# Optimization experiments

Hardware: AMD Instinct MI355X
Metric: run time of the kernel (lower is better)

Reference implementation:

```python
import jax, jax.numpy as jnp
import numpy as np
from jax import lax

B, DIM, H, W = 8, 256, 48, 48
HEADS, DH = 8, 32
K, S = 5, 2
P = K // 2
SCALE = DH ** -0.5
EPS = 1e-5


def setup_inputs() -> dict:
    key = jax.random.key(0)
    ks = jax.random.split(key, 12)
    w = lambda k, sh: jax.random.normal(k, sh, jnp.float32) * 0.02
    return {
        'x': jax.random.normal(ks[0], (B, DIM, H, W), jnp.float32),
        'kv': jax.random.normal(ks[1], (B, DIM, H, W), jnp.float32),
        'wq': w(ks[2], (DIM, DIM)), 'bq': jnp.zeros((DIM,), jnp.float32),
        'wk': w(ks[3], (DIM, DIM)), 'bk': jnp.zeros((DIM,), jnp.float32),
        'wv': w(ks[4], (DIM, DIM)), 'bv': jnp.zeros((DIM,), jnp.float32),
        'w_dw': w(ks[5], (DH, 1, K, K)), 'b_dw': jnp.zeros((DH,), jnp.float32),
        'ln_w': jnp.ones((DH,), jnp.float32), 'ln_b': jnp.zeros((DH,), jnp.float32),
        'w_off': w(ks[6], (2, DH)),
        'wo': w(ks[7], (DIM, DIM)), 'bo': jnp.zeros((DIM,), jnp.float32),
    }


def conv1x1(x, w, b=None):
    # x: (B, Cin, H, W), w: (Cout, Cin)
    y = jnp.einsum('oc,bchw->bohw', w, x)
    return y if b is None else y + b[None, :, None, None]


def grid_sample_bilinear(inp, grid):
    # inp: (N, C, Hh, Ww); grid: (N, Hg, Wg, 2) in (x, y), align_corners=True
    N, C, Hh, Ww = inp.shape
    gx = (grid[..., 0] + 1.0) * 0.5 * (Ww - 1)
    gy = (grid[..., 1] + 1.0) * 0.5 * (Hh - 1)
    x0 = jnp.floor(gx)
    y0 = jnp.floor(gy)
    wx = gx - x0  # frac weights for x1/y1 corners
    wy = gy - y0
    x0i = jnp.clip(x0.astype(jnp.int32), 0, Ww - 1)
    x1i = jnp.clip(x0.astype(jnp.int32) + 1, 0, Ww - 1)
    y0i = jnp.clip(y0.astype(jnp.int32), 0, Hh - 1)
    y1i = jnp.clip(y0.astype(jnp.int32) + 1, 0, Hh - 1)
    flat = inp.reshape(N, C, Hh * Ww)
    n = grid.shape[1] * grid.shape[2]

    def gather(yi, xi):
        idx = (yi * Ww + xi).reshape(N, 1, n)
        return jnp.take_along_axis(flat, jnp.broadcast_to(idx, (N, C, n)), axis=2)

    w00 = ((1 - wx) * (1 - wy)).reshape(N, 1, n)
    w01 = (wx * (1 - wy)).reshape(N, 1, n)
    w10 = ((1 - wx) * wy).reshape(N, 1, n)
    w11 = (wx * wy).reshape(N, 1, n)
    return (w00 * gather(y0i, x0i) + w01 * gather(y0i, x1i)
            + w10 * gather(y1i, x0i) + w11 * gather(y1i, x1i))  # (N, C, n)


def reference(x, kv, wq, bq, wk, bk, wv, bv, w_dw, b_dw, ln_w, ln_b, w_off, wo, bo):
    q = conv1x1(x, wq, bq)                      # (B, DIM, H, W)
    q_off = q.reshape(B * HEADS, DH, H, W)      # per-head channels
    # depthwise offset conv
    t = lax.conv_general_dilated(q_off, w_dw, (S, S), [(P, P), (P, P)],
                                 feature_group_count=DH,
                                 dimension_numbers=('NCHW', 'OIHW', 'NCHW'))
    t = t + b_dw[None, :, None, None]
    Hk, Wk = t.shape[2], t.shape[3]
    n = Hk * Wk
    # LayerNormProxy: LN over channel dim
    t = t.transpose(0, 2, 3, 1)                 # (BH, Hk, Wk, DH)
    mu = t.mean(-1, keepdims=True)
    var = ((t - mu) ** 2).mean(-1, keepdims=True)
    t = (t - mu) / jnp.sqrt(var + EPS) * ln_w + ln_b
    t = jax.nn.gelu(t, approximate=False)
    offset = jnp.einsum('oc,bhwc->bhwo', w_off, t)  # (BH, Hk, Wk, 2) as (y, x)
    # reference points, normalized to [-1, 1]
    ref_y = (jnp.linspace(0.5, Hk - 0.5, Hk, dtype=jnp.float32) / (Hk - 1.0)) * 2.0 - 1.0
    ref_x = (jnp.linspace(0.5, Wk - 0.5, Wk, dtype=jnp.float32) / (Wk - 1.0)) * 2.0 - 1.0
    ref = jnp.stack(jnp.meshgrid(ref_y, ref_x, indexing='ij'), axis=-1)  # (Hk, Wk, 2)
    pos = jnp.clip(offset + ref[None], -1.0, 1.0)
    grid = pos[..., ::-1]                       # (x, y) order for sampling
    kvs = grid_sample_bilinear(kv.reshape(B * HEADS, DH, H, W), grid)  # (BH, DH, n)
    kv4 = kvs.reshape(B, DIM, 1, n)
    k = conv1x1(kv4, wk, bk).reshape(B * HEADS, DH, n)
    v = conv1x1(kv4, wv, bv).reshape(B * HEADS, DH, n)
    qf = q.reshape(B * HEADS, DH, H * W)
    attn = jax.nn.softmax(jnp.einsum('bcm,bcn->bmn', qf, k) * SCALE, axis=2)
    out = jnp.einsum('bmn,bcn->bcm', attn, v).reshape(B, DIM, H, W)
    return conv1x1(out, wo, bo)
```

## Files before the change

kernel.cpp:

```cpp
#include <hip/hip_runtime.h>
#include <hip/hip_bf16.h>
#include <cstddef>

#define BB 8
#define DIM 256
#define HH 48
#define WW 48
#define HW 2304
#define HEADS 8
#define DH 32
#define BH 64
#define HK 24
#define WK 24
#define NN 576
#define SCALE 0.17677669529663687f
#define EPSF 1e-5f

typedef __attribute__((ext_vector_type(8))) short short8;
typedef __attribute__((ext_vector_type(4))) float f32x4;

static __device__ inline short f2bf_s(float f) {
  __hip_bfloat16 h = __float2bfloat16(f);
  return *reinterpret_cast<short*>(&h);
}

static __device__ inline unsigned pkrnd(float a, float b) {
  unsigned ua = __builtin_bit_cast(unsigned, a) + 0x8000u;
  unsigned ub = __builtin_bit_cast(unsigned, b) + 0x8000u;
  return __builtin_amdgcn_perm(ub, ua, 0x07060302);
}

__global__ __launch_bounds__(256) void prep(
    const float* __restrict__ x, const float* __restrict__ wq,
    short* __restrict__ Xh, short* __restrict__ Xl,
    short* __restrict__ Wqh, short* __restrict__ Wql) {
  __shared__ float t[64][65];
  const int bid = blockIdx.x;
  if (bid < 1152) {
    int mt = bid % 36, t2 = bid / 36;
    int ct = t2 & 3, b = t2 >> 2;
    const int c0 = ct * 64, m0 = mt * 64;
    const int col = threadIdx.x & 63, row4 = threadIdx.x >> 6;
    const float* xb = x + ((size_t)b * 256 + c0) * HW + m0;
#pragma unroll
    for (int k = 0; k < 16; k++) {
      int c = row4 + k * 4;
      t[c][col] = xb[(size_t)c * HW + col];
    }
    __syncthreads();
    short* oh = Xh + ((size_t)b * HW + m0) * 256 + c0;
    short* ol = Xl + ((size_t)b * HW + m0) * 256 + c0;
#pragma unroll
    for (int k = 0; k < 16; k++) {
      int m = row4 + k * 4;
      float v = t[col][m];
      unsigned u = __builtin_bit_cast(unsigned, v) & 0xffff0000u;
      float rem = v - __builtin_bit_cast(float, u);
      oh[(size_t)m * 256 + col] = (short)(u >> 16);
      ol[(size_t)m * 256 + col] = (short)(__builtin_bit_cast(unsigned, rem) >> 16);
    }
  } else {
    int e0 = (bid - 1152) * 1024 + threadIdx.x * 4;
    float4 v4 = *(const float4*)(wq + e0);
    float vv[4] = {v4.x, v4.y, v4.z, v4.w};
    union { short s[4]; int2 i2; } Hu, Lu;
#pragma unroll
    for (int j = 0; j < 4; j++) {
      unsigned u = __builtin_bit_cast(unsigned, vv[j]) & 0xffff0000u;
      float rem = vv[j] - __builtin_bit_cast(float, u);
      Hu.s[j] = (short)(u >> 16);
      Lu.s[j] = (short)(__builtin_bit_cast(unsigned, rem) >> 16);
    }
    *(int2*)(Wqh + e0) = Hu.i2;
    *(int2*)(Wql + e0) = Lu.i2;
  }
}

__global__ __launch_bounds__(512) void gemm_q_fused(
    const short* __restrict__ Wh, const short* __restrict__ Wl,
    const float* __restrict__ bias,
    const short* __restrict__ Xh, const short* __restrict__ Xl,
    float* __restrict__ Y,
    const float* __restrict__ kv, float* __restrict__ kvT,
    const float* __restrict__ wk, const float* __restrict__ wv,
    const float* __restrict__ wo,
    short* __restrict__ Wkh, short* __restrict__ Wkl,
    short* __restrict__ Wvh, short* __restrict__ Wvl,
    short* __restrict__ Woh, short* __restrict__ Wol) {
  __shared__ short sB[2][64 * 256];
  const int bid = blockIdx.x;
  const int tid = threadIdx.x;

  if (bid < 288) {
    const int b = bid / 36;
    const int mBase = (bid % 36) * 64;
    const short* srcH = Xh + ((size_t)b * HW + mBase) * 256;
    const short* srcL = Xl + ((size_t)b * HW + mBase) * 256;
#pragma unroll
    for (int it = 0; it < 4; it++) {
      int idx = it * 512 + tid;
      int row = idx >> 5, ck = idx & 31;
      int dst = row * 256 + ((ck ^ (row & 7)) << 3);
      *(short8*)(&sB[0][dst]) = *(const short8*)(srcH + (size_t)row * 256 + ck * 8);
      *(short8*)(&sB[1][dst]) = *(const short8*)(srcL + (size_t)row * 256 + ck * 8);
    }
    __syncthreads();

    const int wave = tid >> 6, lane = tid & 63;
    const int quad = lane >> 4, l15 = lane & 15;
    const int oBase = wave * 32;
    f32x4 acc[2][4] = {};
    for (int kc = 0; kc < 256; kc += 32) {
      short8 ah[2], al[2];
#pragma unroll
      for (int os = 0; os < 2; os++) {
        ah[os] = *(const short8*)(Wh + (size_t)(oBase + os * 16 + l15) * 256 + kc + quad * 8);
        al[os] = *(const short8*)(Wl + (size_t)(oBase + os * 16 + l15) * 256 + kc + quad * 8);
      }
#pragma unroll
      for (int mt = 0; mt < 4; mt++) {
        int row = mt * 16 + l15;
        int off = row * 256 + ((((kc >> 3) + quad) ^ (row & 7)) << 3);
        short8 bh_ = *(const short8*)(&sB[0][off]);
        short8 bl_ = *(const short8*)(&sB[1][off]);
#pragma unroll
        for (int os = 0; os < 2; os++) {
          acc[os][mt] = __builtin_amdgcn_mfma_f32_16x16x32_bf16(ah[os], bh_, acc[os][mt], 0, 0, 0);
          acc[os][mt] = __builtin_amdgcn_mfma_f32_16x16x32_bf16(al[os], bh_, acc[os][mt], 0, 0, 0);
          acc[os][mt] = __builtin_amdgcn_mfma_f32_16x16x32_bf16(ah[os], bl_, acc[os][mt], 0, 0, 0);
        }
      }
    }
#pragma unroll
    for (int os = 0; os < 2; os++)
#pragma unroll
      for (int r = 0; r < 4; r++) {
        int o = oBase + os * 16 + quad * 4 + r;
        float bs = bias[o];
        float* yp = Y + ((size_t)b * 256 + o) * HW + mBase + l15;
#pragma unroll
        for (int mt = 0; mt < 4; mt++) yp[mt * 16] = acc[os][mt][r] + bs;
      }
  } else if (bid < 1440) {
    float* tf = (float*)sB;
    int bb = bid - 288;
    int mt = bb % 36, t2 = bb / 36;
    int ct = t2 & 3, b = t2 >> 2;
    const int c0 = ct * 64, m0 = mt * 64;
    const int col = tid & 63, row8 = tid >> 6;
    const float* xb = kv + ((size_t)b * 256 + c0) * HW + m0;
#pragma unroll
    for (int k = 0; k < 8; k++) {
      int c = row8 + k * 8;
      tf[c * 65 + col] = xb[(size_t)c * HW + col];
    }
    __syncthreads();
    float* ot = kvT + ((size_t)b * HW + m0) * 256 + c0;
#pragma unroll
    for (int k = 0; k < 8; k++) {
      int m = row8 + k * 8;
      ot[(size_t)m * 256 + col] = tf[col * 65 + m];
    }
  } else {
    const float* srcs[3] = {wk, wv, wo};
    short* his[3] = {Wkh, Wvh, Woh};
    short* los[3] = {Wkl, Wvl, Wol};
    int bb = bid - 1440;
    int w = bb >> 5;
    int off = (bb & 31) * 2048 + tid * 4;
    float4 v4 = *(const float4*)(srcs[w] + off);
    float vv[4] = {v4.x, v4.y, v4.z, v4.w};
    union { short s[4]; int2 i2; } Hu, Lu;
#pragma unroll
    for (int j = 0; j < 4; j++) {
      unsigned u = __builtin_bit_cast(unsigned, vv[j]) & 0xffff0000u;
      float rem = vv[j] - __builtin_bit_cast(float, u);
      Hu.s[j] = (short)(u >> 16);
      Lu.s[j] = (short)(__builtin_bit_cast(unsigned, rem) >> 16);
    }
    *(int2*)(his[w] + off) = Hu.i2;
    *(int2*)(los[w] + off) = Lu.i2;
  }
}

#define QPS 101
__global__ __launch_bounds__(256) void dw_sample_kernel(
    const float* __restrict__ q, const float* __restrict__ kvT,
    const float* __restrict__ w_dw, const float* __restrict__ b_dw,
    const float* __restrict__ ln_w, const float* __restrict__ ln_b,
    const float* __restrict__ w_off, short* __restrict__ kvsTh,
    short* __restrict__ kvsTl) {
  __shared__ float s_q[32 * QPS];
  __shared__ float s_w[DH * 25];
  const int tid = threadIdx.x;
  const int ch = tid & 31;
  const int np = tid >> 5;
  const int bid = blockIdx.x;
  const int b = bid & 7;
  const int r = bid >> 3;
  const int head = r / 72;
  const int rr = r - head * 72;
  const int yk = rr / 3;
  const int xk0 = (rr - yk * 3) * 8;
  const int bh = b * 8 + head;
  const int xk = xk0 + np;
  const int n = yk * WK + xk;

  for (int i = tid; i < DH * 25; i += 256) s_w[i] = w_dw[i];

  {
    const int y0 = yk * 2 - 2, x0 = xk0 * 2 - 2;
    const float* qbh = q + (size_t)bh * DH * HW;
#pragma unroll
    for (int it = 0; it < 13; it++) {
      int e = it * 256 + tid;
      if (e < 3200) {
        int c = e / 100;
        int rem = e - c * 100;
        int dy = rem / 20;
        int xl = rem - dy * 20;
        int gy = y0 + dy, gx = x0 + xl;
        float v = 0.f;
        if ((unsigned)gy < HH && (unsigned)gx < WW)
          v = qbh[(size_t)c * HW + gy * WW + gx];
        s_q[c * QPS + dy * 20 + xl] = v;
      }
    }
  }
  __syncthreads();

  float t = b_dw[ch];
  {
    const float* wp = s_w + ch * 25;
    const float* qp = s_q + ch * QPS + np * 2;
#pragma unroll
    for (int dy = 0; dy < 5; dy++)
#pragma unroll
      for (int dx = 0; dx < 5; dx++)
        t += wp[dy * 5 + dx] * qp[dy * 20 + dx];
  }

  float mu = t;
#pragma unroll
  for (int m = 1; m < 32; m <<= 1) mu += __shfl_xor(mu, m);
  mu *= (1.0f / DH);
  float d = t - mu;
  float var = d * d;
#pragma unroll
  for (int m = 1; m < 32; m <<= 1) var += __shfl_xor(var, m);
  var *= (1.0f / DH);
  float rstd = rsqrtf(var + EPSF);

  float xn = d * rstd * ln_w[ch] + ln_b[ch];
  float g = 0.5f * xn * (1.0f + erff(xn * 0.70710678118654752f));
  float o0 = w_off[ch] * g;
  float o1 = w_off[DH + ch] * g;
#pragma unroll
  for (int m = 1; m < 32; m <<= 1) {
    o0 += __shfl_xor(o0, m);
    o1 += __shfl_xor(o1, m);
  }

  const float ref_y = (0.5f + (float)yk) / 23.0f * 2.0f - 1.0f;
  const float ref_x = (0.5f + (float)xk) / 23.0f * 2.0f - 1.0f;
  float py = fminf(fmaxf(o0 + ref_y, -1.0f), 1.0f);
  float px = fminf(fmaxf(o1 + ref_x, -1.0f), 1.0f);

  float gx = (px + 1.0f) * 0.5f * 47.0f;
  float gy = (py + 1.0f) * 0.5f * 47.0f;
  float x0f = floorf(gx), y0f = floorf(gy);
  float wx = gx - x0f, wy = gy - y0f;
  int x0 = (int)x0f, y0 = (int)y0f;
  int x0i = min(max(x0, 0), WW - 1);
  int x1i = min(max(x0 + 1, 0), WW - 1);
  int y0i = min(max(y0, 0), HH - 1);
  int y1i = min(max(y0 + 1, 0), HH - 1);
  float w00 = (1.f - wx) * (1.f - wy);
  float w01 = wx * (1.f - wy);
  float w10 = (1.f - wx) * wy;
  float w11 = wx * wy;

  const float* kvb = kvT + (size_t)b * HW * 256 + head * DH + ch;
  float val = w00 * kvb[(size_t)(y0i * WW + x0i) * 256]
            + w01 * kvb[(size_t)(y0i * WW + x1i) * 256]
            + w10 * kvb[(size_t)(y1i * WW + x0i) * 256]
            + w11 * kvb[(size_t)(y1i * WW + x1i) * 256];

  unsigned ub = __builtin_bit_cast(unsigned, val);
  unsigned uh = ub & 0xffff0000u;
  float rem = val - __builtin_bit_cast(float, uh);
  size_t idx = ((size_t)b * NN + n) * 256 + head * DH + ch;
  kvsTh[idx] = (short)(uh >> 16);
  kvsTl[idx] = (short)(__builtin_bit_cast(unsigned, rem) >> 16);
}

__global__ __launch_bounds__(256) void kv_gemm_mfma(
    const short* __restrict__ Wkh, const short* __restrict__ Wkl,
    const float* __restrict__ bk,
    const short* __restrict__ Wvh, const short* __restrict__ Wvl,
    const float* __restrict__ bv,
    const short* __restrict__ Xh, const short* __restrict__ Xl,
    short* __restrict__ Kb, short* __restrict__ Vb) {
  const int tid = threadIdx.x;
  const int wave = tid >> 6;
  const int lane = tid & 63;
  const int quad = lane >> 4, l15 = lane & 15;
  const int b = blockIdx.z;
  const int mode = blockIdx.y >> 2;
  const int oTile = (blockIdx.y & 3) * 64;
  const int nBase = blockIdx.x * 64;

  if (mode == 0) {
    const int nW = nBase + wave * 16;
    const short* arh = Xh + ((size_t)b * NN + nW + l15) * 256 + quad * 8;
    const short* arl = Xl + ((size_t)b * NN + nW + l15) * 256 + quad * 8;
    f32x4 acc[4] = {};
    for (int kc = 0; kc < 256; kc += 32) {
      short8 ah = *(const short8*)(arh + kc);
      short8 al = *(const short8*)(arl + kc);
#pragma unroll
      for (int ot = 0; ot < 4; ot++) {
        short8 bh_ = *(const short8*)(Wkh + (size_t)(oTile + ot * 16 + l15) * 256 + kc + quad * 8);
        short8 bl_ = *(const short8*)(Wkl + (size_t)(oTile + ot * 16 + l15) * 256 + kc + quad * 8);
        acc[ot] = __builtin_amdgcn_mfma_f32_16x16x32_bf16(ah, bh_, acc[ot], 0, 0, 0);
        acc[ot] = __builtin_amdgcn_mfma_f32_16x16x32_bf16(al, bh_, acc[ot], 0, 0, 0);
        acc[ot] = __builtin_amdgcn_mfma_f32_16x16x32_bf16(ah, bl_, acc[ot], 0, 0, 0);
      }
    }
    float bs[4];
#pragma unroll
    for (int ot = 0; ot < 4; ot++) bs[ot] = bk[oTile + ot * 16 + l15];
#pragma unroll
    for (int r = 0; r < 4; r++) {
      short* yp = Kb + ((size_t)b * NN + nW + quad * 4 + r) * 256 + oTile + l15;
#pragma unroll
      for (int ot = 0; ot < 4; ot++) yp[ot * 16] = f2bf_s(acc[ot][r] + bs[ot]);
    }
  } else {
    const int oW = oTile + wave * 16;
    const short* arh = Wvh + (size_t)(oW + l15) * 256 + quad * 8;
    const short* arl = Wvl + (size_t)(oW + l15) * 256 + quad * 8;
    f32x4 acc[4] = {};
    for (int kc = 0; kc < 256; kc += 32) {
      short8 ah = *(const short8*)(arh + kc);
      short8 al = *(const short8*)(arl + kc);
#pragma unroll
      for (int nt = 0; nt < 4; nt++) {
        short8 bh_ = *(const short8*)(Xh + ((size_t)b * NN + nBase + nt * 16 + l15) * 256 + kc + quad * 8);
        short8 bl_ = *(const short8*)(Xl + ((size_t)b * NN + nBase + nt * 16 + l15) * 256 + kc + quad * 8);
        acc[nt] = __builtin_amdgcn_mfma_f32_16x16x32_bf16(ah, bh_, acc[nt], 0, 0, 0);
        acc[nt] = __builtin_amdgcn_mfma_f32_16x16x32_bf16(al, bh_, acc[nt], 0, 0, 0);
        acc[nt] = __builtin_amdgcn_mfma_f32_16x16x32_bf16(ah, bl_, acc[nt], 0, 0, 0);
      }
    }
#pragma unroll
    for (int r = 0; r < 4; r++) {
      int o = oW + quad * 4 + r;
      float bs = bv[o];
      short* yp = Vb + ((size_t)b * 256 + o) * NN + nBase + l15;
#pragma unroll
      for (int nt = 0; nt < 4; nt++) yp[nt * 16] = f2bf_s(acc[nt][r] + bs);
    }
  }
}

__global__ __launch_bounds__(256) void attn_mfma(const float* __restrict__ q,
                                                 const short* __restrict__ Kb,
                                                 const short* __restrict__ Vb,
                                                 short* __restrict__ O) {
  __shared__ short sK[2][64 * 40];
  __shared__ short sV[2][32 * 88];
  __shared__ int sP[4][2][256];
  const int tid = threadIdx.x;
  const int wave = tid >> 6;
  const int lane = tid & 63;
  const int quad = lane >> 4;
  const int l15 = lane & 15;
  const int bh = blockIdx.y;
  const int b = bh >> 3, head = bh & 7;
  const int mBase = blockIdx.x * 128 + wave * 32;

  short8 bq[2];
#pragma unroll
  for (int mt = 0; mt < 2; mt++) {
    const float* qp = q + ((size_t)bh * DH + quad * 8) * HW + mBase + mt * 16 + l15;
    short8 v;
#pragma unroll
    for (int j = 0; j < 8; j++) v[j] = f2bf_s(qp[(size_t)j * HW] * SCALE);
    bq[mt] = v;
  }

  const int kn = tid >> 2, kc = (tid & 3) * 8;
  const int vc = tid >> 3, vn = (tid & 7) * 8;
  const short* kg = Kb + (size_t)b * NN * 256 + head * DH;
  const short* vg = Vb + ((size_t)b * 256 + head * DH) * NN;

  short8 kreg = *(const short8*)(kg + (size_t)kn * 256 + kc);
  short8 vreg = *(const short8*)(vg + (size_t)vc * NN + vn);
  *(short8*)(&sK[0][kn * 40 + kc]) = kreg;
  *(short8*)(&sV[0][vc * 88 + vn]) = vreg;
  __syncthreads();

  const int g = (l15 >> 1) & 3;
  const int row16 = l15 * 16;
  const int wr0 = row16 + (((quad >> 1) ^ g) << 2) + ((quad & 1) << 1);
  const int wr1 = row16 + (((2 + (quad >> 1)) ^ g) << 2) + ((quad & 1) << 1);
  const int rd = row16 + ((quad ^ g) << 2);

  f32x4 oacc[2][2] = {};
  f32x4 dacc[2] = {};
  const short ONE = 0x3F80;
  const short8 ones = {ONE, ONE, ONE, ONE, ONE, ONE, ONE, ONE};

  for (int s = 0; s < 9; s++) {
    const int buf = s & 1;
    if (s + 1 < 9) {
      kreg = *(const short8*)(kg + (size_t)((s + 1) * 64 + kn) * 256 + kc);
      vreg = *(const short8*)(vg + (size_t)vc * NN + (s + 1) * 64 + vn);
    }
#pragma unroll
    for (int nt = 0; nt < 2; nt++) {
      short8 ka0 = *(const short8*)(&sK[buf][(nt * 32 + l15) * 40 + quad * 8]);
      short8 ka1 = *(const short8*)(&sK[buf][(nt * 32 + 16 + l15) * 40 + quad * 8]);
      short8 va0 = *(const short8*)(&sV[buf][l15 * 88 + nt * 32 + quad * 8]);
      short8 va1 = *(const short8*)(&sV[buf][(16 + l15) * 88 + nt * 32 + quad * 8]);
      f32x4 z = {0.f, 0.f, 0.f, 0.f};
      f32x4 st[2][2];
      st[0][0] = __builtin_amdgcn_mfma_f32_16x16x32_bf16(ka0, bq[0], z, 0, 0, 0);
      st[0][1] = __builtin_amdgcn_mfma_f32_16x16x32_bf16(ka1, bq[0], z, 0, 0, 0);
      st[1][0] = __builtin_amdgcn_mfma_f32_16x16x32_bf16(ka0, bq[1], z, 0, 0, 0);
      st[1][1] = __builtin_amdgcn_mfma_f32_16x16x32_bf16(ka1, bq[1], z, 0, 0, 0);
#pragma unroll
      for (int mt = 0; mt < 2; mt++) {
        float p0 = __expf(st[mt][0][0]), p1 = __expf(st[mt][0][1]);
        float p2 = __expf(st[mt][0][2]), p3 = __expf(st[mt][0][3]);
        float p4 = __expf(st[mt][1][0]), p5 = __expf(st[mt][1][1]);
        float p6 = __expf(st[mt][1][2]), p7 = __expf(st[mt][1][3]);
        int* base = &sP[wave][mt][0];
        *(int2*)(base + wr0) = make_int2((int)pkrnd(p0, p1), (int)pkrnd(p2, p3));
        *(int2*)(base + wr1) = make_int2((int)pkrnd(p4, p5), (int)pkrnd(p6, p7));
      }
#pragma unroll
      for (int mt = 0; mt < 2; mt++) {
        short8 pa = *(short8*)(&sP[wave][mt][0] + rd);
        oacc[mt][0] = __builtin_amdgcn_mfma_f32_16x16x32_bf16(pa, va0, oacc[mt][0], 0, 0, 0);
        oacc[mt][1] = __builtin_amdgcn_mfma_f32_16x16x32_bf16(pa, va1, oacc[mt][1], 0, 0, 0);
        dacc[mt] = __builtin_amdgcn_mfma_f32_16x16x32_bf16(pa, ones, dacc[mt], 0, 0, 0);
      }
    }
    if (s + 1 < 9) {
      *(short8*)(&sK[buf ^ 1][kn * 40 + kc]) = kreg;
      *(short8*)(&sV[buf ^ 1][vc * 88 + vn]) = vreg;
    }
    __syncthreads();
  }

#pragma unroll
  for (int mt = 0; mt < 2; mt++) {
    short* ob = O + ((size_t)b * HW + mBase + mt * 16) * 256 + head * DH + l15;
#pragma unroll
    for (int r = 0; r < 4; r++) {
      float inv = 1.0f / dacc[mt][r];
      ob[(size_t)(quad * 4 + r) * 256] = f2bf_s(oacc[mt][0][r] * inv);
      ob[(size_t)(quad * 4 + r) * 256 + 16] = f2bf_s(oacc[mt][1][r] * inv);
    }
  }
}

__global__ __launch_bounds__(512) void wo_gemm_mfma(const short* __restrict__ Whi,
                                                    const short* __restrict__ Wlo,
                                                    const float* __restrict__ bias,
                                                    const short* __restrict__ X,
                                                    float* __restrict__ Y) {
  __shared__ short sX[64 * 256];
  const int tid = threadIdx.x;
  const int b = blockIdx.y;
  const int mBase = blockIdx.x * 64;

  const short* src = X + ((size_t)b * HW + mBase) * 256;
#pragma unroll
  for (int it = 0; it < 4; it++) {
    int idx = it * 512 + tid;
    int row = idx >> 5, ck = idx & 31;
    *(short8*)(&sX[row * 256 + ((ck ^ (row & 7)) << 3)]) =
        *(const short8*)(src + (size_t)row * 256 + ck * 8);
  }
  __syncthreads();

  const int wave = tid >> 6, lane = tid & 63;
  const int quad = lane >> 4, l15 = lane & 15;
  const int oBase = wave * 32;

  f32x4 acc[2][4] = {};
  for (int kc = 0; kc < 256; kc += 32) {
    short8 ah[2], al[2];
#pragma unroll
    for (int os = 0; os < 2; os++) {
      ah[os] = *(const short8*)(Whi + (size_t)(oBase + os * 16 + l15) * 256 + kc + quad * 8);
      al[os] = *(const short8*)(Wlo + (size_t)(oBase + os * 16 + l15) * 256 + kc + quad * 8);
    }
#pragma unroll
    for (int mt = 0; mt < 4; mt++) {
      int row = mt * 16 + l15;
      short8 bx = *(const short8*)(&sX[row * 256 + ((((kc >> 3) + quad) ^ (row & 7)) << 3)]);
#pragma unroll
      for (int os = 0; os < 2; os++) {
        acc[os][mt] = __builtin_amdgcn_mfma_f32_16x16x32_bf16(ah[os], bx, acc[os][mt], 0, 0, 0);
        acc[os][mt] = __builtin_amdgcn_mfma_f32_16x16x32_bf16(al[os], bx, acc[os][mt], 0, 0, 0);
      }
    }
  }

#pragma unroll
  for (int os = 0; os < 2; os++)
#pragma unroll
    for (int r = 0; r < 4; r++) {
      int o = oBase + os * 16 + quad * 4 + r;
      float bs = bias[o];
      float* yp = Y + ((size_t)b * 256 + o) * HW + mBase + l15;
#pragma unroll
      for (int mt = 0; mt < 4; mt++) yp[mt * 16] = acc[os][mt][r] + bs;
    }
}

extern "C" void kernel_launch(void* const* d_in, const int* in_sizes, int n_in,
                              void* d_out, int out_size, void* d_ws, size_t ws_size,
                              hipStream_t stream) {
  const float* x    = (const float*)d_in[0];
  const float* kv   = (const float*)d_in[1];
  const float* wq   = (const float*)d_in[2];
  const float* bq   = (const float*)d_in[3];
  const float* wk   = (const float*)d_in[4];
  const float* bk   = (const float*)d_in[5];
  const float* wv   = (const float*)d_in[6];
  const float* bv   = (const float*)d_in[7];
  const float* w_dw = (const float*)d_in[8];
  const float* b_dw = (const float*)d_in[9];
  const float* ln_w = (const float*)d_in[10];
  const float* ln_b = (const float*)d_in[11];
  const float* w_off= (const float*)d_in[12];
  const float* wo   = (const float*)d_in[13];
  const float* bo   = (const float*)d_in[14];
  float* out = (float*)d_out;
  float* ws = (float*)d_ws;

  float* q     = ws;
  short* Xth   = (short*)(ws + 4718592);
  short* O     = (short*)(ws + 4718592);
  short* Xtl   = (short*)(ws + 7077888);
  short* kvsTh = (short*)(ws + 7077888);
  short* kvsTl = (short*)(ws + 7667712);
  short* Kb    = (short*)(ws + 8257536);
  short* Vb    = (short*)(ws + 8847360);
  short* Wqh   = (short*)(ws + 9437184);
  short* Wql = Wqh + 65536;
  short* Wkh = Wql + 65536;
  short* Wkl = Wkh + 65536;
  short* Wvh = Wkl + 65536;
  short* Wvl = Wvh + 65536;
  short* Woh = Wvl + 65536;
  short* Wol = Woh + 65536;
  float* kvT = out;

  prep<<<dim3(1216), dim3(256), 0, stream>>>(x, wq, Xth, Xtl, Wqh, Wql);
  gemm_q_fused<<<dim3(1536), dim3(512), 0, stream>>>(
      Wqh, Wql, bq, Xth, Xtl, q,
      kv, kvT, wk, wv, wo, Wkh, Wkl, Wvh, Wvl, Woh, Wol);
  dw_sample_kernel<<<dim3(BH * NN / 8), dim3(256), 0, stream>>>(
      q, kvT, w_dw, b_dw, ln_w, ln_b, w_off, kvsTh, kvsTl);
  kv_gemm_mfma<<<dim3(NN / 64, 8, BB), dim3(256), 0, stream>>>(
      Wkh, Wkl, bk, Wvh, Wvl, bv, kvsTh, kvsTl, Kb, Vb);
  attn_mfma<<<dim3(HW / 128, BH), dim3(256), 0, stream>>>(q, Kb, Vb, O);
  wo_gemm_mfma<<<dim3(HW / 64, BB), dim3(512), 0, stream>>>(Woh, Wol, bo, O, out);
}
```

Baseline: 230.7 us.

## Fuse bf16 hi/lo splitting into GEMM kernels and drop prep kernel

Removes the separate prep kernel. The Q GEMM now reads fp32 x directly, transposes it and splits it into bf16 hi/lo in LDS in two channel halves, prefetching the second half while computing on the first. All weight matrices (wq, wk, wv, wo) are loaded as fp32 and split into hi/lo in registers inside the GEMM kernels instead of being pre-converted. This saves one launch and the round trip of the Xh/Xl intermediates through global memory, at the cost of redundant per-block weight conversion and doubled weight load bytes.

Result: faster. 222.0 us (-3.8%).

```diff
diff --git a/kernel.cpp b/kernel.cpp
--- a/kernel.cpp
+++ b/kernel.cpp
@@ -30,107 +30,113 @@
   return __builtin_amdgcn_perm(ub, ua, 0x07060302);
 }
 
-__global__ __launch_bounds__(256) void prep(
-    const float* __restrict__ x, const float* __restrict__ wq,
-    short* __restrict__ Xh, short* __restrict__ Xl,
-    short* __restrict__ Wqh, short* __restrict__ Wql) {
-  __shared__ float t[64][65];
-  const int bid = blockIdx.x;
-  if (bid < 1152) {
-    int mt = bid % 36, t2 = bid / 36;
-    int ct = t2 & 3, b = t2 >> 2;
-    const int c0 = ct * 64, m0 = mt * 64;
-    const int col = threadIdx.x & 63, row4 = threadIdx.x >> 6;
-    const float* xb = x + ((size_t)b * 256 + c0) * HW + m0;
-#pragma unroll
-    for (int k = 0; k < 16; k++) {
-      int c = row4 + k * 4;
-      t[c][col] = xb[(size_t)c * HW + col];
-    }
-    __syncthreads();
-    short* oh = Xh + ((size_t)b * HW + m0) * 256 + c0;
-    short* ol = Xl + ((size_t)b * HW + m0) * 256 + c0;
-#pragma unroll
-    for (int k = 0; k < 16; k++) {
-      int m = row4 + k * 4;
-      float v = t[col][m];
-      unsigned u = __builtin_bit_cast(unsigned, v) & 0xffff0000u;
-      float rem = v - __builtin_bit_cast(float, u);
-      oh[(size_t)m * 256 + col] = (short)(u >> 16);
-      ol[(size_t)m * 256 + col] = (short)(__builtin_bit_cast(unsigned, rem) >> 16);
-    }
-  } else {
-    int e0 = (bid - 1152) * 1024 + threadIdx.x * 4;
-    float4 v4 = *(const float4*)(wq + e0);
-    float vv[4] = {v4.x, v4.y, v4.z, v4.w};
-    union { short s[4]; int2 i2; } Hu, Lu;
-#pragma unroll
-    for (int j = 0; j < 4; j++) {
-      unsigned u = __builtin_bit_cast(unsigned, vv[j]) & 0xffff0000u;
-      float rem = vv[j] - __builtin_bit_cast(float, u);
-      Hu.s[j] = (short)(u >> 16);
-      Lu.s[j] = (short)(__builtin_bit_cast(unsigned, rem) >> 16);
-    }
-    *(int2*)(Wqh + e0) = Hu.i2;
-    *(int2*)(Wql + e0) = Lu.i2;
-  }
+static __device__ inline void split8(const float* xf, short8& bh, short8& bl) {
+  union { unsigned u[4]; short8 v; } H, L;
+#pragma unroll
+  for (int p = 0; p < 4; p++) {
+    float x0 = xf[2 * p], x1 = xf[2 * p + 1];
+    unsigned u0 = __builtin_bit_cast(unsigned, x0) & 0xffff0000u;
+    unsigned u1 = __builtin_bit_cast(unsigned, x1) & 0xffff0000u;
+    float l0 = x0 - __builtin_bit_cast(float, u0);
+    float l1 = x1 - __builtin_bit_cast(float, u1);
+    H.u[p] = __builtin_amdgcn_perm(u1, u0, 0x07060302);
+    L.u[p] = __builtin_amdgcn_perm(__builtin_bit_cast(unsigned, l1),
+                                   __builtin_bit_cast(unsigned, l0), 0x07060302);
+  }
+  bh = H.v;
+  bl = L.v;
 }
 
 __global__ __launch_bounds__(512) void gemm_q_fused(
-    const short* __restrict__ Wh, const short* __restrict__ Wl,
-    const float* __restrict__ bias,
-    const short* __restrict__ Xh, const short* __restrict__ Xl,
-    float* __restrict__ Y,
-    const float* __restrict__ kv, float* __restrict__ kvT,
-    const float* __restrict__ wk, const float* __restrict__ wv,
-    const float* __restrict__ wo,
-    short* __restrict__ Wkh, short* __restrict__ Wkl,
-    short* __restrict__ Wvh, short* __restrict__ Wvl,
-    short* __restrict__ Woh, short* __restrict__ Wol) {
-  __shared__ short sB[2][64 * 256];
+    const float* __restrict__ wq, const float* __restrict__ bias,
+    const float* __restrict__ x, float* __restrict__ Y,
+    const float* __restrict__ kv, float* __restrict__ kvT) {
+  __shared__ float sLDS[16384];
+  float* s_raw = sLDS;
+  short* s_h   = (short*)(sLDS + 8192);
+  short* s_l   = ((short*)(sLDS + 8192)) + 8192;
   const int bid = blockIdx.x;
   const int tid = threadIdx.x;
 
   if (bid < 288) {
     const int b = bid / 36;
     const int mBase = (bid % 36) * 64;
-    const short* srcH = Xh + ((size_t)b * HW + mBase) * 256;
-    const short* srcL = Xl + ((size_t)b * HW + mBase) * 256;
-#pragma unroll
-    for (int it = 0; it < 4; it++) {
-      int idx = it * 512 + tid;
-      int row = idx >> 5, ck = idx & 31;
-      int dst = row * 256 + ((ck ^ (row & 7)) << 3);
-      *(short8*)(&sB[0][dst]) = *(const short8*)(srcH + (size_t)row * 256 + ck * 8);
-      *(short8*)(&sB[1][dst]) = *(const short8*)(srcL + (size_t)row * 256 + ck * 8);
-    }
-    __syncthreads();
-
     const int wave = tid >> 6, lane = tid & 63;
     const int quad = lane >> 4, l15 = lane & 15;
     const int oBase = wave * 32;
+    const int cm = tid & 63, cg = tid >> 6;
+    const int ck0 = cg * 2, ck1 = cg * 2 + 1;
+    const int cvt0 = cm * 128 + ((ck0 ^ (cm & 7)) << 3);
+    const int cvt1 = cm * 128 + ((ck1 ^ (cm & 7)) << 3);
+
     f32x4 acc[2][4] = {};
-    for (int kc = 0; kc < 256; kc += 32) {
-      short8 ah[2], al[2];
-#pragma unroll
-      for (int os = 0; os < 2; os++) {
-        ah[os] = *(const short8*)(Wh + (size_t)(oBase + os * 16 + l15) * 256 + kc + quad * 8);
-        al[os] = *(const short8*)(Wl + (size_t)(oBase + os * 16 + l15) * 256 + kc + quad * 8);
-      }
-#pragma unroll
-      for (int mt = 0; mt < 4; mt++) {
-        int row = mt * 16 + l15;
-        int off = row * 256 + ((((kc >> 3) + quad) ^ (row & 7)) << 3);
-        short8 bh_ = *(const short8*)(&sB[0][off]);
-        short8 bl_ = *(const short8*)(&sB[1][off]);
+
+    {
+      const float* xb = x + ((size_t)b * 256) * HW + mBase;
+#pragma unroll
+      for (int it = 0; it < 4; it++) {
+        int u = it * 512 + tid;
+        int c = u >> 4, f4 = u & 15;
+        *(float4*)(&s_raw[c * 64 + f4 * 4]) =
+            *(const float4*)(xb + (size_t)c * HW + f4 * 4);
+      }
+    }
+    __syncthreads();
+
+    for (int half = 0; half < 2; half++) {
+      {
+        float vals[16];
+#pragma unroll
+        for (int i = 0; i < 16; i++) vals[i] = s_raw[(cg * 16 + i) * 64 + cm];
+        short8 h0, l0, h1, l1;
+        split8(vals, h0, l0);
+        split8(vals + 8, h1, l1);
+        *(short8*)(&s_h[cvt0]) = h0;
+        *(short8*)(&s_l[cvt0]) = l0;
+        *(short8*)(&s_h[cvt1]) = h1;
+        *(short8*)(&s_l[cvt1]) = l1;
+      }
+      __syncthreads();
+
+      if (half == 0) {
+        const float* xb = x + ((size_t)b * 256 + 128) * HW + mBase;
+#pragma unroll
+        for (int it = 0; it < 4; it++) {
+          int u = it * 512 + tid;
+          int c = u >> 4, f4 = u & 15;
+          *(float4*)(&s_raw[c * 64 + f4 * 4]) =
+              *(const float4*)(xb + (size_t)c * HW + f4 * 4);
+        }
+      }
+
+      for (int kc = 0; kc < 128; kc += 32) {
+        short8 ah[2], al[2];
 #pragma unroll
         for (int os = 0; os < 2; os++) {
-          acc[os][mt] = __builtin_amdgcn_mfma_f32_16x16x32_bf16(ah[os], bh_, acc[os][mt], 0, 0, 0);
-          acc[os][mt] = __builtin_amdgcn_mfma_f32_16x16x32_bf16(al[os], bh_, acc[os][mt], 0, 0, 0);
-          acc[os][mt] = __builtin_amdgcn_mfma_f32_16x16x32_bf16(ah[os], bl_, acc[os][mt], 0, 0, 0);
+          const float* wrow = wq + (size_t)(oBase + os * 16 + l15) * 256 +
+                              half * 128 + kc + quad * 8;
+          float w8[8];
+          *(float4*)(w8) = *(const float4*)(wrow);
+          *(float4*)(w8 + 4) = *(const float4*)(wrow + 4);
+          split8(w8, ah[os], al[os]);
         }
-      }
-    }
+#pragma unroll
+        for (int mt = 0; mt < 4; mt++) {
+          int row = mt * 16 + l15;
+          int off = row * 128 + ((((kc >> 3) + quad) ^ (row & 7)) << 3);
+          short8 bh_ = *(const short8*)(&s_h[off]);
+          short8 bl_ = *(const short8*)(&s_l[off]);
+#pragma unroll
+          for (int os = 0; os < 2; os++) {
+            acc[os][mt] = __builtin_amdgcn_mfma_f32_16x16x32_bf16(ah[os], bh_, acc[os][mt], 0, 0, 0);
+            acc[os][mt] = __builtin_amdgcn_mfma_f32_16x16x32_bf16(al[os], bh_, acc[os][mt], 0, 0, 0);
+            acc[os][mt] = __builtin_amdgcn_mfma_f32_16x16x32_bf16(ah[os], bl_, acc[os][mt], 0, 0, 0);
+          }
+        }
+      }
+      __syncthreads();
+    }
+
 #pragma unroll
     for (int os = 0; os < 2; os++)
 #pragma unroll
@@ -141,8 +147,8 @@
 #pragma unroll
         for (int mt = 0; mt < 4; mt++) yp[mt * 16] = acc[os][mt][r] + bs;
       }
-  } else if (bid < 1440) {
-    float* tf = (float*)sB;
+  } else {
+    float* tf = sLDS;
     int bb = bid - 288;
     int mt = bb % 36, t2 = bb / 36;
     int ct = t2 & 3, b = t2 >> 2;
@@ -161,25 +167,6 @@
       int m = row8 + k * 8;
       ot[(size_t)m * 256 + col] = tf[col * 65 + m];
     }
-  } else {
-    const float* srcs[3] = {wk, wv, wo};
-    short* his[3] = {Wkh, Wvh, Woh};
-    short* los[3] = {Wkl, Wvl, Wol};
-    int bb = bid - 1440;
-    int w = bb >> 5;
-    int off = (bb & 31) * 2048 + tid * 4;
-    float4 v4 = *(const float4*)(srcs[w] + off);
-    float vv[4] = {v4.x, v4.y, v4.z, v4.w};
-    union { short s[4]; int2 i2; } Hu, Lu;
-#pragma unroll
-    for (int j = 0; j < 4; j++) {
-      unsigned u = __builtin_bit_cast(unsigned, vv[j]) & 0xffff0000u;
-      float rem = vv[j] - __builtin_bit_cast(float, u);
-      Hu.s[j] = (short)(u >> 16);
-      Lu.s[j] = (short)(__builtin_bit_cast(unsigned, rem) >> 16);
-    }
-    *(int2*)(his[w] + off) = Hu.i2;
-    *(int2*)(los[w] + off) = Lu.i2;
   }
 }
 
@@ -295,10 +282,8 @@
 }
 
 __global__ __launch_bounds__(256) void kv_gemm_mfma(
-    const short* __restrict__ Wkh, const short* __restrict__ Wkl,
-    const float* __restrict__ bk,
-    const short* __restrict__ Wvh, const short* __restrict__ Wvl,
-    const float* __restrict__ bv,
+    const float* __restrict__ wk, const float* __restrict__ bk,
+    const float* __restrict__ wv, const float* __restrict__ bv,
     const short* __restrict__ Xh, const short* __restrict__ Xl,
     short* __restrict__ Kb, short* __restrict__ Vb) {
   const int tid = threadIdx.x;
@@ -320,8 +305,12 @@
       short8 al = *(const short8*)(arl + kc);
 #pragma unroll
       for (int ot = 0; ot < 4; ot++) {
-        short8 bh_ = *(const short8*)(Wkh + (size_t)(oTile + ot * 16 + l15) * 256 + kc + quad * 8);
-        short8 bl_ = *(const short8*)(Wkl + (size_t)(oTile + ot * 16 + l15) * 256 + kc + quad * 8);
+        const float* wrow = wk + (size_t)(oTile + ot * 16 + l15) * 256 + kc + quad * 8;
+        float w8[8];
+        *(float4*)(w8) = *(const float4*)(wrow);
+        *(float4*)(w8 + 4) = *(const float4*)(wrow + 4);
+        short8 bh_, bl_;
+        split8(w8, bh_, bl_);
         acc[ot] = __builtin_amdgcn_mfma_f32_16x16x32_bf16(ah, bh_, acc[ot], 0, 0, 0);
         acc[ot] = __builtin_amdgcn_mfma_f32_16x16x32_bf16(al, bh_, acc[ot], 0, 0, 0);
         acc[ot] = __builtin_amdgcn_mfma_f32_16x16x32_bf16(ah, bl_, acc[ot], 0, 0, 0);
@@ -338,12 +327,14 @@
     }
   } else {
     const int oW = oTile + wave * 16;
-    const short* arh = Wvh + (size_t)(oW + l15) * 256 + quad * 8;
-    const short* arl = Wvl + (size_t)(oW + l15) * 256 + quad * 8;
+    const float* wrow = wv + (size_t)(oW + l15) * 256 + quad * 8;
     f32x4 acc[4] = {};
     for (int kc = 0; kc < 256; kc += 32) {
-      short8 ah = *(const short8*)(arh + kc);
-      short8 al = *(const short8*)(arl + kc);
+      float w8[8];
+      *(float4*)(w8) = *(const float4*)(wrow + kc);
+      *(float4*)(w8 + 4) = *(const float4*)(wrow + kc + 4);
+      short8 ah, al;
+      split8(w8, ah, al);
 #pragma unroll
       for (int nt = 0; nt < 4; nt++) {
         short8 bh_ = *(const short8*)(Xh + ((size_t)b * NN + nBase + nt * 16 + l15) * 256 + kc + quad * 8);
@@ -467,8 +458,7 @@
   }
 }
 
-__global__ __launch_bounds__(512) void wo_gemm_mfma(const short* __restrict__ Whi,
-                                                    const short* __restrict__ Wlo,
+__global__ __launch_bounds__(512) void wo_gemm_mfma(const float* __restrict__ wo,
                                                     const float* __restrict__ bias,
                                                     const short* __restrict__ X,
                                                     float* __restrict__ Y) {
@@ -496,8 +486,11 @@
     short8 ah[2], al[2];
 #pragma unroll
     for (int os = 0; os < 2; os++) {
-      ah[os] = *(const short8*)(Whi + (size_t)(oBase + os * 16 + l15) * 256 + kc + quad * 8);
-      al[os] = *(const short8*)(Wlo + (size_t)(oBase + os * 16 + l15) * 256 + kc + quad * 8);
+      const float* wrow = wo + (size_t)(oBase + os * 16 + l15) * 256 + kc + quad * 8;
+      float w8[8];
+      *(float4*)(w8) = *(const float4*)(wrow);
+      *(float4*)(w8 + 4) = *(const float4*)(wrow + 4);
+      split8(w8, ah[os], al[os]);
     }
 #pragma unroll
     for (int mt = 0; mt < 4; mt++) {
@@ -545,31 +538,18 @@
   float* ws = (float*)d_ws;
 
   float* q     = ws;
-  short* Xth   = (short*)(ws + 4718592);
   short* O     = (short*)(ws + 4718592);
-  short* Xtl   = (short*)(ws + 7077888);
   short* kvsTh = (short*)(ws + 7077888);
   short* kvsTl = (short*)(ws + 7667712);
   short* Kb    = (short*)(ws + 8257536);
   short* Vb    = (short*)(ws + 8847360);
-  short* Wqh   = (short*)(ws + 9437184);
-  short* Wql = Wqh + 65536;
-  short* Wkh = Wql + 65536;
-  short* Wkl = Wkh + 65536;
-  short* Wvh = Wkl + 65536;
-  short* Wvl = Wvh + 65536;
-  short* Woh = Wvl + 65536;
-  short* Wol = Woh + 65536;
   float* kvT = out;
 
-  prep<<<dim3(1216), dim3(256), 0, stream>>>(x, wq, Xth, Xtl, Wqh, Wql);
-  gemm_q_fused<<<dim3(1536), dim3(512), 0, stream>>>(
-      Wqh, Wql, bq, Xth, Xtl, q,
-      kv, kvT, wk, wv, wo, Wkh, Wkl, Wvh, Wvl, Woh, Wol);
+  gemm_q_fused<<<dim3(1440), dim3(512), 0, stream>>>(wq, bq, x, q, kv, kvT);
   dw_sample_kernel<<<dim3(BH * NN / 8), dim3(256), 0, stream>>>(
       q, kvT, w_dw, b_dw, ln_w, ln_b, w_off, kvsTh, kvsTl);
   kv_gemm_mfma<<<dim3(NN / 64, 8, BB), dim3(256), 0, stream>>>(
-      Wkh, Wkl, bk, Wvh, Wvl, bv, kvsTh, kvsTl, Kb, Vb);
+      wk, bk, wv, bv, kvsTh, kvsTl, Kb, Vb);
   attn_mfma<<<dim3(HW / 128, BH), dim3(256), 0, stream>>>(q, Kb, Vb, O);
-  wo_gemm_mfma<<<dim3(HW / 64, BB), dim3(512), 0, stream>>>(Woh, Wol, bo, O, out);
-}
+  wo_gemm_mfma<<<dim3(HW / 64, BB), dim3(512), 0, stream>>>(wo, bo, O, out);
+}
```
